# Performance work log

Hardware: AMD Instinct MI355X
Metric: run time of the kernel (lower is better)

The kernel has to match this reference:

```python
import jax, jax.numpy as jnp
import numpy as np

B, S, V, E, H, L = 128, 512, 32000, 256, 256, 9


def setup_inputs() -> dict:
    key = jax.random.key(0)
    ks = jax.random.split(key, 12)
    src_input = jax.random.randint(ks[0], (B, S), 0, V, dtype=jnp.int32)
    labels = jax.random.randint(ks[1], (B, S), 0, L, dtype=jnp.int32)
    masks = jnp.ones((B, S), dtype=bool)  # torchcrf requires mask[:, 0] all True
    g = lambda k, shape, s: (jax.random.normal(k, shape, jnp.float32) * s)
    inv = 1.0 / np.sqrt(H)
    return {
        "src_input": src_input,
        "labels": labels,
        "masks": masks,
        "embedding": g(ks[2], (V, E), 0.1),
        "W_ih": g(ks[3], (4 * H, E), inv),
        "W_hh": g(ks[4], (4 * H, H), inv),
        "b_ih": g(ks[5], (4 * H,), inv),
        "b_hh": g(ks[6], (4 * H,), inv),
        "W_lin": g(ks[7], (L, H), inv),
        "b_lin": g(ks[8], (L,), inv),
        "start_trans": g(ks[9], (L,), 0.1),
        "end_trans": g(ks[10], (L,), 0.1),
        "trans": g(ks[11], (L, L), 0.1),
    }


def _lstm(x, W_ih, W_hh, b_ih, b_hh):
    # x: [B,S,E] -> hidden states [B,S,H]; PyTorch gate order i,f,g,o
    b, s, _ = x.shape
    h_dim = W_hh.shape[1]
    xp = jnp.einsum('bse,ge->sbg', x, W_ih) + b_ih  # [S,B,4H] precomputed input proj

    def step(carry, xt):
        h, c = carry
        gates = xt + h @ W_hh.T + b_hh
        i, f, g, o = jnp.split(gates, 4, axis=-1)
        c = jax.nn.sigmoid(f) * c + jax.nn.sigmoid(i) * jnp.tanh(g)
        h = jax.nn.sigmoid(o) * jnp.tanh(c)
        return (h, c), h

    h0 = jnp.zeros((b, h_dim), x.dtype)
    _, hs = jax.lax.scan(step, (h0, h0), xp)  # [S,B,H]
    return jnp.swapaxes(hs, 0, 1)


def _crf_nll(emissions, labels, masks, start_trans, end_trans, trans):
    # torchcrf log-likelihood (reduction='sum'); model returns its negation
    maskf = masks.astype(emissions.dtype)
    lab = labels.astype(jnp.int32)
    # numerator: score of gold path
    em_tag = jnp.take_along_axis(emissions, lab[..., None], axis=2)[..., 0]  # [B,S]
    trans_sc = trans[lab[:, :-1], lab[:, 1:]]  # [B,S-1]
    score = start_trans[lab[:, 0]] + em_tag[:, 0]
    score = score + jnp.sum((trans_sc + em_tag[:, 1:]) * maskf[:, 1:], axis=1)
    seq_ends = jnp.sum(masks.astype(jnp.int32), axis=1) - 1
    last_tags = jnp.take_along_axis(lab, seq_ends[:, None], axis=1)[:, 0]
    score = score + end_trans[last_tags]
    # denominator: forward algorithm (log partition)
    alpha0 = start_trans + emissions[:, 0]  # [B,L]
    em_t = jnp.swapaxes(emissions, 0, 1)[1:]  # [S-1,B,L]
    m_t = jnp.swapaxes(masks, 0, 1)[1:]  # [S-1,B]

    def step(alpha, inp):
        e, m = inp
        nxt = jax.nn.logsumexp(alpha[:, :, None] + trans[None] + e[:, None, :], axis=1)
        return jnp.where(m[:, None], nxt, alpha), None

    alphaT, _ = jax.lax.scan(step, alpha0, (em_t, m_t))
    logZ = jax.nn.logsumexp(alphaT + end_trans, axis=1)  # [B]
    return -jnp.sum(score - logZ)


def reference(src_input, labels, masks, embedding, W_ih, W_hh, b_ih, b_hh,
              W_lin, b_lin, start_trans, end_trans, trans):
    x = embedding[src_input]  # [B,S,E]
    hs = _lstm(x, W_ih, W_hh, b_ih, b_hh)  # [B,S,H]; dropout is identity in eval
    emissions = jax.nn.relu(hs) @ W_lin.T + b_lin  # [B,S,L]
    return _crf_nll(emissions, labels, masks, start_trans, end_trans, trans)
```

## Files before the change

### kernel.cpp

```cpp
#include <hip/hip_runtime.h>
#include <hip/hip_fp16.h>
#include <stdint.h>

#define B_ 128
#define S_ 512
#define E_ 256
#define H_ 256
#define G_ 1024
#define L_ 9

#define NREG 52
#define NLDS 12
#define WREG_U4 (NREG * 512)
#define WTOT_U4 (WREG_U4 + NLDS * 512)

#define SM_WL_BYTES (NLDS * 512 * 16)
#define SM_H2       SM_WL_BYTES
#define SMEM2_TOTAL (SM_WL_BYTES + 1024)

#define WS_W      0
#define WS_XP     (512 * 1024)
#define WS_HS     (WS_XP + (size_t)S_ * B_ * G_ * 2)
#define WS_EMB16  (WS_HS + (size_t)S_ * B_ * H_ * 2)
#define WS_WIH16  (WS_EMB16 + (size_t)32000 * E_ * 2)

typedef _Float16 f16x8v __attribute__((ext_vector_type(8)));
typedef float    f32x4v __attribute__((ext_vector_type(4)));

__device__ __forceinline__ uint32_t pack_f16x2(float a, float b) {
    __half2 h = __floats2half2_rn(a, b);
    union { __half2 h2; uint32_t u; } c;
    c.h2 = h;
    return c.u;
}

__device__ __forceinline__ float dot2h(uint32_t w, uint32_t h, float acc) {
#if __has_builtin(__builtin_amdgcn_fdot2)
    typedef _Float16 h2v __attribute__((ext_vector_type(2)));
    union { uint32_t u; h2v v; } uw, uh;
    uw.u = w; uh.u = h;
    return __builtin_amdgcn_fdot2(uw.v, uh.v, acc, false);
#else
    union { uint32_t u; __half2 h2; } uw, uh;
    uw.u = w; uh.u = h;
    float2 wf = __half22float2(uw.h2);
    float2 hf = __half22float2(uh.h2);
    return fmaf(wf.y, hf.y, fmaf(wf.x, hf.x, acc));
#endif
}

__device__ __forceinline__ float dot4h(uint4 w, uint4 h, float acc) {
    acc = dot2h(w.x, h.x, acc);
    acc = dot2h(w.y, h.y, acc);
    acc = dot2h(w.z, h.z, acc);
    acc = dot2h(w.w, h.w, acc);
    return acc;
}

__device__ __forceinline__ float sigm(float x)  { return 1.f / (1.f + __expf(-x)); }
__device__ __forceinline__ float tanh_f(float x){ return 1.f - 2.f / (__expf(2.f * x) + 1.f); }

__device__ __forceinline__ void lds_barrier() {
    asm volatile("s_waitcnt lgkmcnt(0)\n\ts_barrier" ::: "memory");
}

__global__ __launch_bounds__(256) void prep_weights(const float* __restrict__ W_hh,
                                                    uint4* __restrict__ W) {
    int idx = blockIdx.x * 256 + threadIdx.x;
    int l = idx & 63, w = (idx >> 6) & 7, q;
    if (idx < WREG_U4) q = (idx >> 9) + NLDS;
    else               q = (idx - WREG_U4) >> 9;
    int kt = q >> 3, nt = q & 7;
    int gate = nt & 3, jbl = nt >> 2;
    int jb = 2 * w + jbl;
    int row = gate * 256 + jb * 16 + (l & 15);
    int col = kt * 32 + (l >> 4) * 8;
    const float* p = W_hh + (size_t)row * H_ + col;
    uint4 v;
    v.x = pack_f16x2(p[0], p[1]);
    v.y = pack_f16x2(p[2], p[3]);
    v.z = pack_f16x2(p[4], p[5]);
    v.w = pack_f16x2(p[6], p[7]);
    W[idx] = v;
}

__global__ __launch_bounds__(256) void cvt_f16(const float* __restrict__ in,
                                               uint4* __restrict__ out, int n8) {
    int i = blockIdx.x * 256 + threadIdx.x;
    if (i >= n8) return;
    const float4* p = (const float4*)(in + (size_t)i * 8);
    float4 a = p[0], b = p[1];
    uint4 v;
    v.x = pack_f16x2(a.x, a.y);
    v.y = pack_f16x2(a.z, a.w);
    v.z = pack_f16x2(b.x, b.y);
    v.w = pack_f16x2(b.z, b.w);
    out[i] = v;
}

#define LDK 264
__global__ __launch_bounds__(256, 2) void xp_gemm_mfma(
    const int* __restrict__ src, const __half* __restrict__ emb16,
    const __half* __restrict__ wih16, const float* __restrict__ b_ih,
    const float* __restrict__ b_hh, __half* __restrict__ xp16)
{
    __shared__ __align__(16) __half A_lds[64 * LDK];
    __shared__ __align__(16) __half Bt_lds[64 * LDK];
    __shared__ __align__(16) __half C_lds[64 * 72];
    __shared__ int tok[64];
    __shared__ float bias[64];

    int tid = threadIdx.x;
    int r0  = blockIdx.x * 64;
    int j0  = blockIdx.y * 16;

    if (tid < 64) {
        int r = r0 + tid;
        int tt = r >> 7, bb = r & 127;
        tok[tid] = src[bb * S_ + tt];
        int grow = (tid >> 4) * 256 + j0 + (tid & 15);
        bias[tid] = b_ih[grow] + b_hh[grow];
    }
    __syncthreads();

    #pragma unroll
    for (int jl = 0; jl < 8; ++jl) {
        int f = jl * 256 + tid;
        int row = f >> 5, c16 = f & 31;
        const uint4* ap = (const uint4*)(emb16 + (size_t)tok[row] * E_) + c16;
        int growb = (row >> 4) * 256 + j0 + (row & 15);
        const uint4* bp = (const uint4*)(wih16 + (size_t)growb * E_) + c16;
        *(uint4*)&A_lds[row * LDK + c16 * 8]  = *ap;
        *(uint4*)&Bt_lds[row * LDK + c16 * 8] = *bp;
    }
    __syncthreads();

    int lane = tid & 63, w = tid >> 6;
    int ln = lane & 15, quad = lane >> 4;

    f32x4v acc0 = {0.f, 0.f, 0.f, 0.f};
    f32x4v acc1 = {0.f, 0.f, 0.f, 0.f};
    f32x4v acc2 = {0.f, 0.f, 0.f, 0.f};
    f32x4v acc3 = {0.f, 0.f, 0.f, 0.f};

    #pragma unroll
    for (int kc = 0; kc < 8; ++kc) {
        int ko = kc * 32 + quad * 8;
        f16x8v af  = *(const f16x8v*)&A_lds[(w * 16 + ln) * LDK + ko];
        f16x8v bf0 = *(const f16x8v*)&Bt_lds[(ln)      * LDK + ko];
        f16x8v bf1 = *(const f16x8v*)&Bt_lds[(16 + ln) * LDK + ko];
        f16x8v bf2 = *(const f16x8v*)&Bt_lds[(32 + ln) * LDK + ko];
        f16x8v bf3 = *(const f16x8v*)&Bt_lds[(48 + ln) * LDK + ko];
        acc0 = __builtin_amdgcn_mfma_f32_16x16x32_f16(af, bf0, acc0, 0, 0, 0);
        acc1 = __builtin_amdgcn_mfma_f32_16x16x32_f16(af, bf1, acc1, 0, 0, 0);
        acc2 = __builtin_amdgcn_mfma_f32_16x16x32_f16(af, bf2, acc2, 0, 0, 0);
        acc3 = __builtin_amdgcn_mfma_f32_16x16x32_f16(af, bf3, acc3, 0, 0, 0);
    }
    __syncthreads();

    #pragma unroll
    for (int nt = 0; nt < 4; ++nt) {
        f32x4v a = (nt == 0) ? acc0 : (nt == 1) ? acc1 : (nt == 2) ? acc2 : acc3;
        float bs = bias[nt * 16 + ln];
        #pragma unroll
        for (int reg = 0; reg < 4; ++reg) {
            int ml = w * 16 + quad * 4 + reg;
            C_lds[ml * 72 + ln * 4 + nt] = __float2half(a[reg] + bs);
        }
    }
    __syncthreads();

    int orow = tid >> 2, oc = tid & 3;
    uint4 vv = *(const uint4*)&C_lds[orow * 72 + oc * 16];
    *(uint4*)(xp16 + (size_t)(r0 + orow) * G_ + j0 * 4 + oc * 16) = vv;
}

__global__ __launch_bounds__(512, 2) void lstm_rec(
    const uint4* __restrict__ Wv, const __half* __restrict__ xp16,
    __half* __restrict__ hs)
{
    extern __shared__ char smem[];
    uint4*  wlds = (uint4*)smem;
    __half* hbuf = (__half*)(smem + SM_H2);

    int b    = blockIdx.x;
    int tid  = threadIdx.x;
    int l    = tid & 63, w = tid >> 6;
    int quad = l >> 4, ln = l & 15;

    f16x8v wr[NREG];
    #pragma unroll
    for (int q = 0; q < NREG; ++q)
        wr[q] = *(const f16x8v*)&Wv[q * 512 + tid];
    #pragma unroll
    for (int tl = 0; tl < NLDS; ++tl)
        wlds[w * (NLDS * 64) + tl * 64 + l] = Wv[WREG_U4 + tl * 512 + tid];

    if (tid < 256) hbuf[tid] = __float2half(0.f);
    __syncthreads();

    float c0 = 0.f, c1 = 0.f;
    const __half* xbase = xp16 + (size_t)b * G_;
    int j0 = 32 * w + ln;
    int j1 = j0 + 16;
    __half* ho = hs + (size_t)b * S_ * H_;
    const uint4* wp = wlds + (size_t)w * (NLDS * 64) + l;

    const f32x4v zz = {0.f, 0.f, 0.f, 0.f};
    uint2 xa = *(const uint2*)(xbase + j0 * 4);
    uint2 xb = *(const uint2*)(xbase + j0 * 4 + 64);

    for (int t = 0; t < S_; ++t) {
        int cur = t & 1, nxt = cur ^ 1;
        const __half* hb = hbuf + cur * 256 + quad * 8;

        f32x4v acc[8];
        f16x8v a = *(const f16x8v*)(hb);
        #pragma unroll
        for (int kt = 0; kt < 8; ++kt) {
            f16x8v anx = a;
            if (kt < 7) anx = *(const f16x8v*)(hb + (kt + 1) * 32);
            #pragma unroll
            for (int nt = 0; nt < 8; ++nt) {
                int q = kt * 8 + nt;
                f16x8v bf;
                if (q < NLDS) bf = *(const f16x8v*)&wp[q * 64];
                else          bf = wr[q - NLDS];
                f32x4v cin = (kt == 0) ? zz : acc[nt];
                acc[nt] = __builtin_amdgcn_mfma_f32_16x16x32_f16(a, bf, cin, 0, 0, 0);
            }
            a = anx;
        }

        union { uint32_t u; __half2 h2; } u0, u1;
        u0.u = xa.x; u1.u = xa.y;
        float2 fa = __half22float2(u0.h2);
        float2 fb = __half22float2(u1.h2);
        float pi = acc[0][0] + fa.x, pf = acc[1][0] + fa.y;
        float pg = acc[2][0] + fb.x, po = acc[3][0] + fb.y;
        c0 = sigm(pf) * c0 + sigm(pi) * tanh_f(pg);
        float h0 = sigm(po) * tanh_f(c0);

        u0.u = xb.x; u1.u = xb.y;
        fa = __half22float2(u0.h2);
        fb = __half22float2(u1.h2);
        pi = acc[4][0] + fa.x; pf = acc[5][0] + fa.y;
        pg = acc[6][0] + fb.x; po = acc[7][0] + fb.y;
        c1 = sigm(pf) * c1 + sigm(pi) * tanh_f(pg);
        float h1 = sigm(po) * tanh_f(c1);

        if (quad == 0) {
            hbuf[nxt * 256 + j0] = __float2half(h0);
            hbuf[nxt * 256 + j1] = __float2half(h1);
        } else if (quad == 1) {
            ho[(size_t)t * H_ + j0] = __float2half(fmaxf(h0, 0.f));
            ho[(size_t)t * H_ + j1] = __float2half(fmaxf(h1, 0.f));
        }

        xbase += (size_t)B_ * G_;
        uint2 na = *(const uint2*)(xbase + j0 * 4);
        uint2 nb = *(const uint2*)(xbase + j0 * 4 + 64);

        lds_barrier();
        xa = na; xb = nb;
    }
}

__global__ __launch_bounds__(256) void emis_crf(
    const __half* __restrict__ hs, const int* __restrict__ labels,
    const float* __restrict__ W_lin, const float* __restrict__ b_lin,
    const float* __restrict__ start_trans, const float* __restrict__ end_trans,
    const float* __restrict__ trans, float* __restrict__ out)
{
    __shared__ uint32_t wlin2[L_ * 128];
    __shared__ float em_lds[S_ * 10];
    __shared__ int   lab_lds[S_];
    __shared__ float trans_lds[81];
    __shared__ float blin[L_], st_l[L_], en_l[L_];
    __shared__ float alpha_lds[2 * L_];

    int b = blockIdx.x, tid = threadIdx.x;

    for (int i = tid; i < L_ * 128; i += 256) {
        int l = i >> 7, k = i & 127;
        wlin2[i] = pack_f16x2(W_lin[l * H_ + 2 * k], W_lin[l * H_ + 2 * k + 1]);
    }
    if (tid < 81) trans_lds[tid] = trans[tid];
    if (tid < L_) { blin[tid] = b_lin[tid]; st_l[tid] = start_trans[tid]; en_l[tid] = end_trans[tid]; }
    lab_lds[tid]       = labels[b * S_ + tid];
    lab_lds[tid + 256] = labels[b * S_ + tid + 256];
    __syncthreads();

    const uint4* wl4 = (const uint4*)wlin2;
    #pragma unroll
    for (int r = 0; r < 2; ++r) {
        int t = tid + r * 256;
        const uint4* hr = (const uint4*)(hs + ((size_t)b * S_ + t) * H_);
        float acc[L_];
        #pragma unroll
        for (int l = 0; l < L_; ++l) acc[l] = blin[l];
        #pragma unroll
        for (int c = 0; c < 4; ++c) {
            uint4 hreg[8];
            #pragma unroll
            for (int k = 0; k < 8; ++k) hreg[k] = hr[c * 8 + k];
            #pragma unroll
            for (int l = 0; l < L_; ++l) {
                float a = acc[l];
                #pragma unroll
                for (int k = 0; k < 8; ++k)
                    a = dot4h(wl4[l * 32 + c * 8 + k], hreg[k], a);
                acc[l] = a;
            }
        }
        #pragma unroll
        for (int l = 0; l < L_; ++l) em_lds[t * 10 + l] = acc[l];
    }
    __syncthreads();

    if (tid < 16) {
        float score = 0.f;
        int prev_lab = 0;
        if (tid < L_) alpha_lds[tid] = st_l[tid] + em_lds[0 * 10 + tid];
        if (tid == 0) {
            int cl = lab_lds[0];
            prev_lab = cl;
            score = st_l[cl] + em_lds[0 * 10 + cl];
        }
        for (int t = 1; t < S_; ++t) {
            int cu = t & 1, pv = cu ^ 1;
            if (tid < L_) {
                float m = -1e30f;
                #pragma unroll
                for (int i2 = 0; i2 < L_; ++i2)
                    m = fmaxf(m, alpha_lds[pv * L_ + i2] + trans_lds[i2 * L_ + tid]);
                float s = 0.f;
                #pragma unroll
                for (int i2 = 0; i2 < L_; ++i2)
                    s += __expf(alpha_lds[pv * L_ + i2] + trans_lds[i2 * L_ + tid] - m);
                alpha_lds[cu * L_ + tid] = em_lds[t * 10 + tid] + m + __logf(s);
            }
            if (tid == 0) {
                int cl = lab_lds[t];
                score += trans_lds[prev_lab * L_ + cl] + em_lds[t * 10 + cl];
                prev_lab = cl;
            }
        }
        if (tid == 0) {
            int pv = (S_ - 1) & 1;
            float m = -1e30f;
            #pragma unroll
            for (int i2 = 0; i2 < L_; ++i2)
                m = fmaxf(m, alpha_lds[pv * L_ + i2] + en_l[i2]);
            float s = 0.f;
            #pragma unroll
            for (int i2 = 0; i2 < L_; ++i2)
                s += __expf(alpha_lds[pv * L_ + i2] + en_l[i2] - m);
            float logZ = m + __logf(s);
            score += en_l[prev_lab];
            atomicAdd(out, logZ - score);
        }
    }
}

extern "C" void kernel_launch(void* const* d_in, const int* in_sizes, int n_in,
                              void* d_out, int out_size, void* d_ws, size_t ws_size,
                              hipStream_t stream) {
    const int*   src         = (const int*)d_in[0];
    const int*   labels      = (const int*)d_in[1];
    const float* emb         = (const float*)d_in[3];
    const float* W_ih        = (const float*)d_in[4];
    const float* W_hh        = (const float*)d_in[5];
    const float* b_ih        = (const float*)d_in[6];
    const float* b_hh        = (const float*)d_in[7];
    const float* W_lin       = (const float*)d_in[8];
    const float* b_lin       = (const float*)d_in[9];
    const float* start_trans = (const float*)d_in[10];
    const float* end_trans   = (const float*)d_in[11];
    const float* trans       = (const float*)d_in[12];

    uint4*    W     = (uint4*)  ((char*)d_ws + WS_W);
    __half*   xp16  = (__half*) ((char*)d_ws + WS_XP);
    __half*   hsb   = (__half*) ((char*)d_ws + WS_HS);
    __half*   emb16 = (__half*) ((char*)d_ws + WS_EMB16);
    __half*   wih16 = (__half*) ((char*)d_ws + WS_WIH16);

    hipFuncSetAttribute((const void*)lstm_rec,
                        hipFuncAttributeMaxDynamicSharedMemorySize, SMEM2_TOTAL);

    hipMemsetAsync(d_out, 0, sizeof(float), stream);
    prep_weights<<<WTOT_U4 / 256, 256, 0, stream>>>(W_hh, W);
    cvt_f16<<<(32000 * E_ / 8 + 255) / 256, 256, 0, stream>>>(emb, (uint4*)emb16, 32000 * E_ / 8);
    cvt_f16<<<(G_ * E_ / 8 + 255) / 256, 256, 0, stream>>>(W_ih, (uint4*)wih16, G_ * E_ / 8);
    dim3 g1(1024, 16);
    xp_gemm_mfma<<<g1, 256, 0, stream>>>(src, emb16, wih16, b_ih, b_hh, xp16);
    lstm_rec<<<B_, 512, SMEM2_TOTAL, stream>>>(W, xp16, hsb);
    emis_crf<<<B_, 256, 0, stream>>>(hsb, labels, W_lin, b_lin,
                                     start_trans, end_trans, trans, (float*)d_out);
}
```

Before: 1.420 ms.

## Batch 16 sequences per LSTM block and keep all recurrent weights in registers

The recurrent kernel now maps 16 batch rows onto the MFMA M dimension per block, launching 8 blocks instead of 128, so the MFMA rows are no longer mostly wasted. All 64 weight fragments are loaded into registers, half pinned to AGPRs via inline asm, which removes the per-step LDS weight reads. The hidden state buffer becomes a padded 16-row tile. In exchange, each thread performs four times more gate math per step, and far fewer CUs are occupied.

```diff
diff --git a/kernel.cpp b/kernel.cpp
--- a/kernel.cpp
+++ b/kernel.cpp
@@ -9,14 +9,10 @@
 #define G_ 1024
 #define L_ 9
 
-#define NREG 52
-#define NLDS 12
-#define WREG_U4 (NREG * 512)
-#define WTOT_U4 (WREG_U4 + NLDS * 512)
-
-#define SM_WL_BYTES (NLDS * 512 * 16)
-#define SM_H2       SM_WL_BYTES
-#define SMEM2_TOTAL (SM_WL_BYTES + 1024)
+#define WTOT_U4 (8 * 64 * 64)
+
+#define HPAD 258
+#define HBUF_HALF (16 * HPAD)
 
 #define WS_W      0
 #define WS_XP     (512 * 1024)
@@ -26,6 +22,10 @@
 
 typedef _Float16 f16x8v __attribute__((ext_vector_type(8)));
 typedef float    f32x4v __attribute__((ext_vector_type(4)));
+
+__device__ __forceinline__ f16x8v as_f16x8(uint4 v) {
+    union { uint4 u; f16x8v f; } c; c.u = v; return c.f;
+}
 
 __device__ __forceinline__ uint32_t pack_f16x2(float a, float b) {
     __half2 h = __floats2half2_rn(a, b);
@@ -67,13 +67,12 @@
 __global__ __launch_bounds__(256) void prep_weights(const float* __restrict__ W_hh,
                                                     uint4* __restrict__ W) {
     int idx = blockIdx.x * 256 + threadIdx.x;
-    int l = idx & 63, w = (idx >> 6) & 7, q;
-    if (idx < WREG_U4) q = (idx >> 9) + NLDS;
-    else               q = (idx - WREG_U4) >> 9;
+    int l = idx & 63;
+    int q = (idx >> 6) & 63;
+    int w = idx >> 12;
     int kt = q >> 3, nt = q & 7;
     int gate = nt & 3, jbl = nt >> 2;
-    int jb = 2 * w + jbl;
-    int row = gate * 256 + jb * 16 + (l & 15);
+    int row = gate * 256 + (2 * w + jbl) * 16 + (l & 15);
     int col = kt * 32 + (l >> 4) * 8;
     const float* p = W_hh + (size_t)row * H_ + col;
     uint4 v;
@@ -175,94 +174,111 @@
     *(uint4*)(xp16 + (size_t)(r0 + orow) * G_ + j0 * 4 + oc * 16) = vv;
 }
 
+#define LOADW(i) uint4 W##i = wb[(i) * 64]
+#define PINA(i)  asm volatile("" : "+a"(W##i.x), "+a"(W##i.y), "+a"(W##i.z), "+a"(W##i.w))
+#define PINV(i)  asm volatile("" : "+v"(W##i.x), "+v"(W##i.y), "+v"(W##i.z), "+v"(W##i.w))
+#define MM(i, a, c)  c = __builtin_amdgcn_mfma_f32_16x16x32_f16(a, as_f16x8(W##i), c,  0, 0, 0)
+#define MMZ(i, a, c) c = __builtin_amdgcn_mfma_f32_16x16x32_f16(a, as_f16x8(W##i), zz, 0, 0, 0)
+
 __global__ __launch_bounds__(512, 2) void lstm_rec(
     const uint4* __restrict__ Wv, const __half* __restrict__ xp16,
     __half* __restrict__ hs)
 {
-    extern __shared__ char smem[];
-    uint4*  wlds = (uint4*)smem;
-    __half* hbuf = (__half*)(smem + SM_H2);
-
-    int b    = blockIdx.x;
-    int tid  = threadIdx.x;
-    int l    = tid & 63, w = tid >> 6;
+    __shared__ __align__(16) __half hbuf[2 * HBUF_HALF];
+
+    int b0  = blockIdx.x * 16;
+    int tid = threadIdx.x;
+    int l   = tid & 63, w = tid >> 6;
     int quad = l >> 4, ln = l & 15;
 
-    f16x8v wr[NREG];
-    #pragma unroll
-    for (int q = 0; q < NREG; ++q)
-        wr[q] = *(const f16x8v*)&Wv[q * 512 + tid];
-    #pragma unroll
-    for (int tl = 0; tl < NLDS; ++tl)
-        wlds[w * (NLDS * 64) + tl * 64 + l] = Wv[WREG_U4 + tl * 512 + tid];
-
-    if (tid < 256) hbuf[tid] = __float2half(0.f);
-    __syncthreads();
-
-    float c0 = 0.f, c1 = 0.f;
-    const __half* xbase = xp16 + (size_t)b * G_;
-    int j0 = 32 * w + ln;
-    int j1 = j0 + 16;
-    __half* ho = hs + (size_t)b * S_ * H_;
-    const uint4* wp = wlds + (size_t)w * (NLDS * 64) + l;
-
+    const uint4* wb = Wv + (size_t)w * (64 * 64) + l;
+    LOADW(0);  LOADW(1);  LOADW(2);  LOADW(3);  LOADW(4);  LOADW(5);  LOADW(6);  LOADW(7);
+    LOADW(8);  LOADW(9);  LOADW(10); LOADW(11); LOADW(12); LOADW(13); LOADW(14); LOADW(15);
+    LOADW(16); LOADW(17); LOADW(18); LOADW(19); LOADW(20); LOADW(21); LOADW(22); LOADW(23);
+    LOADW(24); LOADW(25); LOADW(26); LOADW(27); LOADW(28); LOADW(29); LOADW(30); LOADW(31);
+    LOADW(32); LOADW(33); LOADW(34); LOADW(35); LOADW(36); LOADW(37); LOADW(38); LOADW(39);
+    LOADW(40); LOADW(41); LOADW(42); LOADW(43); LOADW(44); LOADW(45); LOADW(46); LOADW(47);
+    LOADW(48); LOADW(49); LOADW(50); LOADW(51); LOADW(52); LOADW(53); LOADW(54); LOADW(55);
+    LOADW(56); LOADW(57); LOADW(58); LOADW(59); LOADW(60); LOADW(61); LOADW(62); LOADW(63);
+    PINA(0);  PINA(1);  PINA(2);  PINA(3);  PINA(4);  PINA(5);  PINA(6);  PINA(7);
+    PINA(8);  PINA(9);  PINA(10); PINA(11); PINA(12); PINA(13); PINA(14); PINA(15);
+    PINA(16); PINA(17); PINA(18); PINA(19); PINA(20); PINA(21); PINA(22); PINA(23);
+    PINA(24); PINA(25); PINA(26); PINA(27); PINA(28); PINA(29); PINA(30); PINA(31);
+    PINV(32); PINV(33); PINV(34); PINV(35); PINV(36); PINV(37); PINV(38); PINV(39);
+    PINV(40); PINV(41); PINV(42); PINV(43); PINV(44); PINV(45); PINV(46); PINV(47);
+    PINV(48); PINV(49); PINV(50); PINV(51); PINV(52); PINV(53); PINV(54); PINV(55);
+    PINV(56); PINV(57); PINV(58); PINV(59); PINV(60); PINV(61); PINV(62); PINV(63);
+
+    for (int i = tid; i < 2 * HBUF_HALF; i += 512)
+        hbuf[i] = __float2half(0.f);
+    __syncthreads();
+
+    float c_[8] = {0.f, 0.f, 0.f, 0.f, 0.f, 0.f, 0.f, 0.f};
     const f32x4v zz = {0.f, 0.f, 0.f, 0.f};
-    uint2 xa = *(const uint2*)(xbase + j0 * 4);
-    uint2 xb = *(const uint2*)(xbase + j0 * 4 + 64);
+
+    const __half* xbase = xp16 + (size_t)(b0 + quad * 4) * G_ + (32 * w + ln) * 4;
+    __half* hsb = hs + (size_t)(b0 + quad * 4) * S_ * H_ + 32 * w + ln;
 
     for (int t = 0; t < S_; ++t) {
         int cur = t & 1, nxt = cur ^ 1;
-        const __half* hb = hbuf + cur * 256 + quad * 8;
-
+
+        uint2 xv[8];
+        const __half* xt = xbase + (size_t)t * (B_ * G_);
+        #pragma unroll
+        for (int jb = 0; jb < 2; ++jb)
+            #pragma unroll
+            for (int r = 0; r < 4; ++r)
+                xv[jb * 4 + r] = *(const uint2*)(xt + (size_t)r * G_ + jb * 64);
+
+        const __half* hbc = hbuf + cur * HBUF_HALF + ln * HPAD + quad * 8;
         f32x4v acc[8];
-        f16x8v a = *(const f16x8v*)(hb);
-        #pragma unroll
-        for (int kt = 0; kt < 8; ++kt) {
-            f16x8v anx = a;
-            if (kt < 7) anx = *(const f16x8v*)(hb + (kt + 1) * 32);
-            #pragma unroll
-            for (int nt = 0; nt < 8; ++nt) {
-                int q = kt * 8 + nt;
-                f16x8v bf;
-                if (q < NLDS) bf = *(const f16x8v*)&wp[q * 64];
-                else          bf = wr[q - NLDS];
-                f32x4v cin = (kt == 0) ? zz : acc[nt];
-                acc[nt] = __builtin_amdgcn_mfma_f32_16x16x32_f16(a, bf, cin, 0, 0, 0);
+        f16x8v a;
+        a = *(const f16x8v*)(hbc);
+        MMZ(0, a, acc[0]);  MMZ(1, a, acc[1]);  MMZ(2, a, acc[2]);  MMZ(3, a, acc[3]);
+        MMZ(4, a, acc[4]);  MMZ(5, a, acc[5]);  MMZ(6, a, acc[6]);  MMZ(7, a, acc[7]);
+        a = *(const f16x8v*)(hbc + 32);
+        MM(8, a, acc[0]);   MM(9, a, acc[1]);   MM(10, a, acc[2]);  MM(11, a, acc[3]);
+        MM(12, a, acc[4]);  MM(13, a, acc[5]);  MM(14, a, acc[6]);  MM(15, a, acc[7]);
+        a = *(const f16x8v*)(hbc + 64);
+        MM(16, a, acc[0]);  MM(17, a, acc[1]);  MM(18, a, acc[2]);  MM(19, a, acc[3]);
+        MM(20, a, acc[4]);  MM(21, a, acc[5]);  MM(22, a, acc[6]);  MM(23, a, acc[7]);
+        a = *(const f16x8v*)(hbc + 96);
+        MM(24, a, acc[0]);  MM(25, a, acc[1]);  MM(26, a, acc[2]);  MM(27, a, acc[3]);
+        MM(28, a, acc[4]);  MM(29, a, acc[5]);  MM(30, a, acc[6]);  MM(31, a, acc[7]);
+        a = *(const f16x8v*)(hbc + 128);
+        MM(32, a, acc[0]);  MM(33, a, acc[1]);  MM(34, a, acc[2]);  MM(35, a, acc[3]);
+        MM(36, a, acc[4]);  MM(37, a, acc[5]);  MM(38, a, acc[6]);  MM(39, a, acc[7]);
+        a = *(const f16x8v*)(hbc + 160);
+        MM(40, a, acc[0]);  MM(41, a, acc[1]);  MM(42, a, acc[2]);  MM(43, a, acc[3]);
+        MM(44, a, acc[4]);  MM(45, a, acc[5]);  MM(46, a, acc[6]);  MM(47, a, acc[7]);
+        a = *(const f16x8v*)(hbc + 192);
+        MM(48, a, acc[0]);  MM(49, a, acc[1]);  MM(50, a, acc[2]);  MM(51, a, acc[3]);
+        MM(52, a, acc[4]);  MM(53, a, acc[5]);  MM(54, a, acc[6]);  MM(55, a, acc[7]);
+        a = *(const f16x8v*)(hbc + 224);
+        MM(56, a, acc[0]);  MM(57, a, acc[1]);  MM(58, a, acc[2]);  MM(59, a, acc[3]);
+        MM(60, a, acc[4]);  MM(61, a, acc[5]);  MM(62, a, acc[6]);  MM(63, a, acc[7]);
+
+        __half* hw = hbuf + nxt * HBUF_HALF + (quad * 4) * HPAD + 32 * w + ln;
+        #pragma unroll
+        for (int jb = 0; jb < 2; ++jb) {
+            #pragma unroll
+            for (int r = 0; r < 4; ++r) {
+                int cell = jb * 4 + r;
+                union { uint32_t u; __half2 h2; } u0, u1;
+                u0.u = xv[cell].x; u1.u = xv[cell].y;
+                float2 f01 = __half22float2(u0.h2);
+                float2 f23 = __half22float2(u1.h2);
+                float pi = acc[jb * 4 + 0][r] + f01.x;
+                float pf = acc[jb * 4 + 1][r] + f01.y;
+                float pg = acc[jb * 4 + 2][r] + f23.x;
+                float po = acc[jb * 4 + 3][r] + f23.y;
+                c_[cell] = sigm(pf) * c_[cell] + sigm(pi) * tanh_f(pg);
+                float h = sigm(po) * tanh_f(c_[cell]);
+                hw[r * HPAD + jb * 16] = __float2half(h);
+                hsb[((size_t)r * S_ + t) * H_ + jb * 16] = __float2half(fmaxf(h, 0.f));
             }
-            a = anx;
-        }
-
-        union { uint32_t u; __half2 h2; } u0, u1;
-        u0.u = xa.x; u1.u = xa.y;
-        float2 fa = __half22float2(u0.h2);
-        float2 fb = __half22float2(u1.h2);
-        float pi = acc[0][0] + fa.x, pf = acc[1][0] + fa.y;
-        float pg = acc[2][0] + fb.x, po = acc[3][0] + fb.y;
-        c0 = sigm(pf) * c0 + sigm(pi) * tanh_f(pg);
-        float h0 = sigm(po) * tanh_f(c0);
-
-        u0.u = xb.x; u1.u = xb.y;
-        fa = __half22float2(u0.h2);
-        fb = __half22float2(u1.h2);
-        pi = acc[4][0] + fa.x; pf = acc[5][0] + fa.y;
-        pg = acc[6][0] + fb.x; po = acc[7][0] + fb.y;
-        c1 = sigm(pf) * c1 + sigm(pi) * tanh_f(pg);
-        float h1 = sigm(po) * tanh_f(c1);
-
-        if (quad == 0) {
-            hbuf[nxt * 256 + j0] = __float2half(h0);
-            hbuf[nxt * 256 + j1] = __float2half(h1);
-        } else if (quad == 1) {
-            ho[(size_t)t * H_ + j0] = __float2half(fmaxf(h0, 0.f));
-            ho[(size_t)t * H_ + j1] = __float2half(fmaxf(h1, 0.f));
-        }
-
-        xbase += (size_t)B_ * G_;
-        uint2 na = *(const uint2*)(xbase + j0 * 4);
-        uint2 nb = *(const uint2*)(xbase + j0 * 4 + 64);
-
+        }
         lds_barrier();
-        xa = na; xb = nb;
     }
 }
 
@@ -385,16 +401,13 @@
     __half*   emb16 = (__half*) ((char*)d_ws + WS_EMB16);
     __half*   wih16 = (__half*) ((char*)d_ws + WS_WIH16);
 
-    hipFuncSetAttribute((const void*)lstm_rec,
-                        hipFuncAttributeMaxDynamicSharedMemorySize, SMEM2_TOTAL);
-
     hipMemsetAsync(d_out, 0, sizeof(float), stream);
     prep_weights<<<WTOT_U4 / 256, 256, 0, stream>>>(W_hh, W);
     cvt_f16<<<(32000 * E_ / 8 + 255) / 256, 256, 0, stream>>>(emb, (uint4*)emb16, 32000 * E_ / 8);
     cvt_f16<<<(G_ * E_ / 8 + 255) / 256, 256, 0, stream>>>(W_ih, (uint4*)wih16, G_ * E_ / 8);
     dim3 g1(1024, 16);
     xp_gemm_mfma<<<g1, 256, 0, stream>>>(src, emb16, wih16, b_ih, b_hh, xp16);
-    lstm_rec<<<B_, 512, SMEM2_TOTAL, stream>>>(W, xp16, hsb);
+    lstm_rec<<<8, 512, 0, stream>>>(W, xp16, hsb);
     emis_crf<<<B_, 256, 0, stream>>>(hsb, labels, W_lin, b_lin,
                                      start_trans, end_trans, trans, (float*)d_out);
 }
```

Result: slower. 4.615 ms (+225.0%).
